# Optimization experiments

Measured on AMD Instinct MI355X. Metric: run time of the kernel, lower is better.

## Reference

```python
import math
import jax, jax.numpy as jnp
import numpy as np

P = 8; K = 9; RC = 8; FC = 768; TOPK = 2
THR = 0.2; TEMP = 0.08; DIL = 5; MIX = 0.65; OPEN = 5


def _build_bank():
    axis = np.linspace(-1.0, 1.0, K, dtype=np.float32)
    yy, xx = np.meshgrid(axis, axis, indexing='ij')
    Ls = [0.45, 0.75, 1.05]; Ws = [0.14, 0.2, 0.28]
    kernels, oris, lens, wids = [], [], [], []
    for i in range(P):
        ang = 2.0 * math.pi * i / P
        L = Ls[i % 3]; W = Ws[(i // 3) % 3]
        xr = xx * math.cos(ang) + yy * math.sin(ang)
        yr = -xx * math.sin(ang) + yy * math.cos(ang)
        taper = (1.0 - np.clip(np.abs(xr) / L, 0.0, 1.0)) ** 1.5
        core = np.exp(-0.5 * ((xr / L) ** 2 + (yr / W) ** 2))
        ridge = taper * core * np.clip(1.0 - (yr / W) ** 2, 0.0, None)
        k = ridge - ridge.mean()
        k = k / max(np.abs(k).sum(), 1e-6)
        kernels.append(k.astype(np.float32)); oris.append(ang); lens.append(L); wids.append(W)
    return (jnp.asarray(np.stack(kernels)[:, None]),
            jnp.asarray(np.array(oris, np.float32)),
            jnp.asarray(np.array(lens, np.float32)),
            jnp.asarray(np.array(wids, np.float32)))


def _conv(x, w, b, pad):
    y = jax.lax.conv_general_dilated(x, w, (1, 1), [(pad, pad), (pad, pad)],
                                     dimension_numbers=('NCHW', 'OIHW', 'NCHW'))
    return y + b[None, :, None, None]


def _avg3(x):  # torch avg_pool2d k=3,s=1,p=1 with count_include_pad=True -> sum/9
    s = jax.lax.reduce_window(x, 0.0, jax.lax.add, (1, 1, 3, 3), (1, 1, 1, 1),
                              [(0, 0), (0, 0), (1, 1), (1, 1)])
    return s / 9.0


def _maxp(x, k):
    p = k // 2
    return jax.lax.reduce_window(x, -jnp.inf, jax.lax.max, (1, 1, k, k), (1, 1, 1, 1),
                                 [(0, 0), (0, 0), (p, p), (p, p)])


def _binary_open(mask, k):
    eroded = 1.0 - _maxp(1.0 - mask, k)
    return jnp.clip(_maxp(eroded, k), 0.0, 1.0)


def _normalize(t):
    mn = t.min(axis=(-2, -1), keepdims=True)
    mx = t.max(axis=(-2, -1), keepdims=True)
    return (t - mn) / jnp.maximum(mx - mn, 1e-6)


def _gelu(x):
    return jax.nn.gelu(x, approximate=False)


def _forward(feature_map, theta, length, width, curvature, alpha, objectness,
             prototype_logits, fp1_w, fp1_b, fp2_w, fp2_b, pm1_w, pm1_b,
             pm2_w, pm2_b, proto_delta):
    bank, ori, la, wa = _build_bank()
    carrier = _gelu(_conv(_gelu(_conv(feature_map, fp1_w, fp1_b, 0)), fp2_w, fp2_b, 1))
    carrier_mean = carrier.mean(axis=1, keepdims=True)
    carrier_hp = carrier_mean - _avg3(carrier_mean)
    kernels = bank + 0.05 * proto_delta
    responses = jax.lax.conv_general_dilated(carrier_hp, kernels, (1, 1),
                                             [(K // 2, K // 2)] * 2,
                                             dimension_numbers=('NCHW', 'OIHW', 'NCHW'))
    theta_angle = jnp.tanh(theta) * math.pi  # [B,1,H,W]
    theta_score = jnp.cos(theta_angle - ori[None, :, None, None])
    length_value = jax.nn.sigmoid(length) * 0.85 + 0.25
    width_value = jax.nn.sigmoid(width) * 0.22 + 0.08
    length_score = -(length_value - la[None, :, None, None]) ** 2 / 0.08
    width_score = -(width_value - wa[None, :, None, None]) ** 2 / 0.01
    bias = prototype_logits + 1.25 * theta_score + length_score + width_score
    pw = jax.nn.softmax(bias, axis=1)  # [B,P,H,W]
    # per-pixel top-k prototype selection
    pwt = jnp.moveaxis(pw, 1, -1)  # [B,H,W,P]
    vals, idx = jax.lax.top_k(pwt, TOPK)
    sparse = (jax.nn.one_hot(idx, P, dtype=pw.dtype) * vals[..., None]).sum(axis=-2)
    sparse = sparse / jnp.maximum(sparse.sum(axis=-1, keepdims=True), 1e-6)
    pw = jnp.moveaxis(sparse, -1, 1)
    alpha_map = jax.nn.sigmoid(alpha)
    objectness_map = jax.nn.sigmoid(objectness)
    curvature_map = jnp.tanh(curvature)
    ss = (responses * pw).sum(axis=1, keepdims=True)
    ss = ss - _avg3(ss)
    density = jnp.abs(carrier).mean(axis=1, keepdims=True)
    density = density / jnp.maximum(density.mean(axis=(2, 3), keepdims=True), 1e-6)
    dx = jnp.cos(theta_angle); dy = jnp.sin(theta_angle)
    blob = _avg3(objectness_map)
    # support gating (enabled, hard-mask + opening)
    carrier_support = _normalize(_avg3(jnp.abs(carrier_hp)))
    density_support = _normalize(density)
    ev = MIX * carrier_support + (1.0 - MIX) * density_support
    gate = jax.nn.sigmoid((ev - THR) / TEMP)
    gate = _maxp(gate, DIL)
    mask = (ev >= THR).astype(feature_map.dtype)
    mask = _binary_open(mask, OPEN)
    mask = _maxp(mask, DIL)
    gate = gate * mask
    blob = blob * jax.lax.stop_gradient(gate)
    stroke_gate = alpha_map * blob * (0.7 + 0.3 * jnp.clip(density, 0.0, 2.0))
    ss = stroke_gate * ss * (1.0 + 0.15 * curvature_map)
    feats = jnp.concatenate([carrier * ss, ss, dx * ss, dy * ss, curvature_map * ss], axis=1)  # [B,RC+4,H,W]
    h = _gelu(_conv(feats, pm1_w, pm1_b, 0))
    return _conv(h, pm2_w, pm2_b, 0)  # [B,FC,H,W]


def setup_inputs() -> dict:
    key = jax.random.key(0)
    ks = jax.random.split(key, 16)
    B, H, W = 8, 64, 64
    n = lambda k, s: jax.random.normal(k, s, dtype=jnp.float32)
    return {
        'feature_map': n(ks[0], (B, FC, H, W)),
        'theta': n(ks[1], (B, 1, H, W)),
        'length': n(ks[2], (B, 1, H, W)),
        'width': n(ks[3], (B, 1, H, W)),
        'curvature': n(ks[4], (B, 1, H, W)),
        'alpha': n(ks[5], (B, 1, H, W)),
        'objectness': n(ks[6], (B, 1, H, W)),
        'prototype_logits': n(ks[7], (B, P, H, W)),
        'fp1_w': n(ks[8], (RC, FC, 1, 1)) * 0.02,
        'fp1_b': jnp.zeros((RC,), jnp.float32),
        'fp2_w': n(ks[9], (RC, RC, 3, 3)) * 0.05,
        'fp2_b': jnp.zeros((RC,), jnp.float32),
        'pm1_w': n(ks[10], (RC, RC + 4, 1, 1)) * 0.05,
        'pm1_b': jnp.zeros((RC,), jnp.float32),
        'pm2_w': n(ks[11], (FC, RC, 1, 1)) * 0.05,
        'pm2_b': jnp.zeros((FC,), jnp.float32),
        'proto_delta': n(ks[12], (P, 1, K, K)) * 0.02,
    }


def reference(feature_map, theta, length, width, curvature, alpha, objectness,
              prototype_logits, fp1_w, fp1_b, fp2_w, fp2_b, pm1_w, pm1_b,
              pm2_w, pm2_b, proto_delta):
    return _forward(feature_map, theta, length, width, curvature, alpha, objectness,
                    prototype_logits, fp1_w, fp1_b, fp2_w, fp2_b, pm1_w, pm1_b,
                    pm2_w, pm2_b, proto_delta)
```

## Files before the change

### kernel.cpp

```cpp
#include <hip/hip_runtime.h>
#include <math.h>

#define PI_F 3.14159265358979323846f

__device__ __forceinline__ float gelu_f(float x){ return 0.5f*x*(1.0f+erff(x*0.7071067811865475f)); }
__device__ __forceinline__ float sigm_f(float x){ return 1.0f/(1.0f+expf(-x)); }

typedef float nf4 __attribute__((ext_vector_type(4)));
__device__ __forceinline__ float4 nt_load4(const float4* p){
    nf4 v = __builtin_nontemporal_load((const nf4*)p);
    return make_float4(v.x, v.y, v.z, v.w);
}
__device__ __forceinline__ void nt_store4(float4* p, float4 v){
    nf4 w; w.x=v.x; w.y=v.y; w.z=v.z; w.w=v.w;
    __builtin_nontemporal_store(w, (nf4*)p);
}


__global__ void __launch_bounds__(256) k_conv1(const float* __restrict__ fm,
                        const float* __restrict__ w1, const float* __restrict__ pd,
                        float* __restrict__ part, float* __restrict__ klg){
    int chunk = blockIdx.x;
    int g = blockIdx.y;
    int tid = threadIdx.x;
    __shared__ float wl[96*8];
    __shared__ float4 comb[8][128];
    for (int i=tid;i<768;i+=256){ int c=i>>3, co=i&7; wl[i]=w1[co*768 + g*96 + c]; }
    __syncthreads();
    int b = chunk>>3;
    int f4 = tid&127, half = tid>>7;
    int q0 = ((chunk&7)<<7) + f4;
    const float4* fm4 = (const float4*)fm;
    float4 acc[8];
    #pragma unroll
    for(int co=0;co<8;co++) acc[co]=make_float4(0.f,0.f,0.f,0.f);
    int basec = b*768 + g*96 + half*48;
    #pragma unroll 4
    for(int c=0;c<48;c++){
        float4 x = nt_load4(&fm4[(size_t)(basec+c)*1024 + q0]);
        int ch = half*48 + c;
        #pragma unroll
        for(int co=0;co<8;co++){
            float wv = wl[(ch<<3)+co];
            acc[co].x += wv*x.x; acc[co].y += wv*x.y; acc[co].z += wv*x.z; acc[co].w += wv*x.w;
        }
    }
    if(half==1){
        #pragma unroll
        for(int co=0;co<8;co++) comb[co][f4]=acc[co];
    }
    __syncthreads();
    if(half==0){
        float4* p4 = (float4*)part;
        int gq = (b<<10) + q0;
        #pragma unroll
        for(int co=0;co<8;co++){
            float4 o = comb[co][f4];
            o.x+=acc[co].x; o.y+=acc[co].y; o.z+=acc[co].z; o.w+=acc[co].w;
            p4[(size_t)((g<<3)+co)*8192 + gq] = o;
        }
    }

    if(chunk==0 && g==0){
        __shared__ float ridge[648];
        __shared__ float pmS[8], pdenS[8];
        for(int t=tid;t<648;t+=256){
            int p=t/81, idx=t-p*81;
            int i=idx/9, j=idx-i*9;
            float ay=-1.f+0.25f*(float)i;
            float ax=-1.f+0.25f*(float)j;
            float ang=2.f*PI_F*(float)p*0.125f;
            const float Ls[3]={0.45f,0.75f,1.05f};
            const float Ws[3]={0.14f,0.20f,0.28f};
            float L=Ls[p%3], Wd=Ws[(p/3)%3];
            float cs=cosf(ang), sn=sinf(ang);
            float xr=ax*cs+ay*sn;
            float yr=-ax*sn+ay*cs;
            float tp=1.f-fminf(fabsf(xr)/L,1.f);
            float taper=powf(tp,1.5f);
            float core=expf(-0.5f*((xr/L)*(xr/L)+(yr/Wd)*(yr/Wd)));
            ridge[t]=taper*core*fmaxf(1.f-(yr/Wd)*(yr/Wd),0.f);
        }
        __syncthreads();
        {
            int p=tid>>5, k=tid&31;
            float s=0.f;
            for(int e=k;e<81;e+=32) s+=ridge[p*81+e];
            for(int off=16;off>0;off>>=1) s+=__shfl_down(s,off,32);
            if(k==0) pmS[p]=s*(1.f/81.f);
        }
        __syncthreads();
        {
            int p=tid>>5, k=tid&31;
            float m=pmS[p];
            float s=0.f;
            for(int e=k;e<81;e+=32) s+=fabsf(ridge[p*81+e]-m);
            for(int off=16;off>0;off>>=1) s+=__shfl_down(s,off,32);
            if(k==0) pdenS[p]=fmaxf(s,1e-6f);
        }
        __syncthreads();
        for(int t=tid;t<648;t+=256){
            int p=t/81;
            klg[t]=(ridge[t]-pmS[p])/pdenS[p]+0.05f*pd[t];
        }
    }
}

__global__ void __launch_bounds__(256) k_conv2(const float* __restrict__ part,
    const float* __restrict__ b1, const float* __restrict__ w2, const float* __restrict__ b2,
    float* __restrict__ carrier, float* __restrict__ cm, float* __restrict__ absc,
    float* __restrict__ bpart){
    __shared__ float t1T[8][3][64];
    __shared__ float w2s[576];
    __shared__ float b1s[8];
    __shared__ float sumS[4][64];
    __shared__ float saS[4][64];
    int tid=threadIdx.x, bl=blockIdx.x;
    int b=bl>>6, y=bl&63;
    for(int i=tid;i<576;i+=256) w2s[i]=w2[i];
    if(tid<8) b1s[tid]=b1[tid];
    __syncthreads();
    for(int j=tid;j<1536;j+=256){
        int ci=j/192, rem=j-ci*192, r=rem>>6, x=rem&63;
        int gy=y-1+r;
        float v=0.f;
        if(gy>=0 && gy<64){
            int px=(b<<12)+(gy<<6)+x;
            float s=0.f;
            #pragma unroll
            for(int g=0;g<8;g++) s+=part[(size_t)((g<<3)+ci)*32768+px];
            v=gelu_f(s+b1s[ci]);
        }
        t1T[ci][r][x]=v;
    }
    __syncthreads();
    int x=tid&63, cg=tid>>6;
    float acc[2];
    #pragma unroll
    for(int qq=0;qq<2;qq++) acc[qq]=b2[cg*2+qq];
    for(int ci=0;ci<8;ci++){
        #pragma unroll
        for(int r=0;r<3;r++){
            #pragma unroll
            for(int dx=-1;dx<=1;dx++){
                int xx=x+dx;
                float v=(xx>=0&&xx<64)?t1T[ci][r][xx]:0.f;
                int ti=r*3+(dx+1);
                #pragma unroll
                for(int qq=0;qq<2;qq++) acc[qq]+=v*w2s[(((cg*2+qq)*8+ci)*9)+ti];
            }
        }
    }
    float s2=0.f, sa2=0.f;
    #pragma unroll
    for(int qq=0;qq<2;qq++){
        float cv=gelu_f(acc[qq]);
        carrier[((size_t)((b<<3)+cg*2+qq)<<12)+(y<<6)+x]=cv;
        s2+=cv; sa2+=fabsf(cv);
    }
    sumS[cg][x]=s2; saS[cg][x]=sa2;
    __syncthreads();
    if(cg==0){
        float cmv=(sumS[0][x]+sumS[1][x]+sumS[2][x]+sumS[3][x])*0.125f;
        float av =(saS[0][x]+saS[1][x]+saS[2][x]+saS[3][x])*0.125f;
        int gp=(b<<12)+(y<<6)+x;
        cm[gp]=cmv;
        absc[gp]=av;
        float s=av, mn=av, mx=av;
        #pragma unroll
        for(int off=32;off>0;off>>=1){
            s += __shfl_down(s,off);
            mn = fminf(mn,__shfl_down(mn,off));
            mx = fmaxf(mx,__shfl_down(mx,off));
        }
        if(x==0){
            bpart[bl*8+0]=s;
            bpart[bl*8+3]=mn;
            bpart[bl*8+4]=mx;
        }
    }
}

__global__ void __launch_bounds__(256) k_resp(const float* __restrict__ cm,
    const float* __restrict__ klg, const float* __restrict__ theta,
    const float* __restrict__ length, const float* __restrict__ width,
    const float* __restrict__ plog,
    float* __restrict__ csraw, float* __restrict__ ss0, float* __restrict__ bpart){
    __shared__ float cmT[704];
    __shared__ float chpT[576];
    __shared__ float klS[648];
    __shared__ float mg[64][16];
    int tid=threadIdx.x, bl=blockIdx.x;
    int b=bl>>6, y=bl&63;
    for(int i=tid;i<648;i+=256) klS[i]=klg[i];
    for(int j=tid;j<704;j+=256){
        int r=j>>6, x=j&63;
        int gy=y-5+r;
        cmT[j]=(gy>=0&&gy<64)?cm[(b<<12)+(gy<<6)+x]:0.f;
    }
    __syncthreads();
    for(int j=tid;j<576;j+=256){
        int rh=j>>6, x=j&63;
        int gy=y-4+rh;
        float v=0.f;
        if(gy>=0&&gy<64){
            float s=0.f;
            #pragma unroll
            for(int dy=0;dy<3;dy++){
                #pragma unroll
                for(int dx=-1;dx<=1;dx++){
                    int xx=x+dx;
                    if(xx>=0&&xx<64) s+=cmT[(rh+dy)*64+xx];
                }
            }
            v=cmT[(rh+1)*64+x]-s*(1.f/9.f);
        }
        chpT[j]=v;
    }
    __syncthreads();
    int x=tid&63, qg=tid>>6;
    int gp=(b<<12)+(y<<6)+x;
    float acc[2]={0.f,0.f};
    float cs=0.f;
    for(int dy=-4;dy<=4;dy++){
        int lr=dy+4;
        for(int dx=-4;dx<=4;dx++){
            int xx=x+dx;
            float v=(xx>=0&&xx<64)?chpT[lr*64+xx]:0.f;
            int ti=lr*9+(dx+4);
            acc[0]+=v*klS[(qg*2)*81+ti];
            acc[1]+=v*klS[(qg*2+1)*81+ti];
            if(qg==0 && dy>=-1&&dy<=1&&dx>=-1&&dx<=1) cs+=fabsf(v);
        }
    }
    float ta=tanhf(theta[gp])*PI_F;
    float lv=sigm_f(length[gp])*0.85f+0.25f;
    float wv=sigm_f(width[gp])*0.22f+0.08f;
    const float Ls[3]={0.45f,0.75f,1.05f};
    const float Ws[3]={0.14f,0.20f,0.28f};
    int pp=(y<<6)+x;
    float bias[2];
    #pragma unroll
    for(int qq=0;qq<2;qq++){
        int q=qg*2+qq;
        float ang=2.f*PI_F*(float)q*0.125f;
        float la=Ls[q%3], wa=Ws[(q/3)%3];
        bias[qq]=plog[((size_t)((b<<3)+q)<<12)+pp]
               +1.25f*cosf(ta-ang)
               -(lv-la)*(lv-la)*(1.f/0.08f)
               -(wv-wa)*(wv-wa)*(1.f/0.01f);
    }
    float m1,r1,m2,r2;
    if(bias[1]>bias[0]){ m1=bias[1];r1=acc[1]; m2=bias[0];r2=acc[0]; }
    else               { m1=bias[0];r1=acc[0]; m2=bias[1];r2=acc[1]; }
    mg[x][qg*4+0]=m1; mg[x][qg*4+1]=r1; mg[x][qg*4+2]=m2; mg[x][qg*4+3]=r2;
    __syncthreads();
    if(qg==0){
        float M1=mg[x][0],R1=mg[x][1],M2=mg[x][2],R2=mg[x][3];
        #pragma unroll
        for(int g=1;g<4;g++){
            float m1b=mg[x][g*4],r1b=mg[x][g*4+1],m2b=mg[x][g*4+2],r2b=mg[x][g*4+3];
            if(m1b>M1){
                float nM2,nR2;
                if(m2b>M1){nM2=m2b;nR2=r2b;} else {nM2=M1;nR2=R1;}
                M1=m1b;R1=r1b;M2=nM2;R2=nR2;
            } else if(m1b>M2){
                M2=m1b;R2=r1b;
            }
        }
        float e2=expf(M2-M1);
        float inv=1.0f/(1.0f+e2);
        ss0[gp]=R1*inv + R2*e2*inv;
        float csv=cs*(1.f/9.f);
        csraw[gp]=csv;
        float mn=csv, mx=csv;
        #pragma unroll
        for(int off=32;off>0;off>>=1){
            mn=fminf(mn,__shfl_down(mn,off));
            mx=fmaxf(mx,__shfl_down(mx,off));
        }
        if(x==0){
            bpart[bl*8+1]=mn;
            bpart[bl*8+2]=mx;
        }
    }
}

__global__ void __launch_bounds__(256) k_gate(const float* __restrict__ csraw,
    const float* __restrict__ absc, const float* __restrict__ objn,
    const float* __restrict__ alpha, const float* __restrict__ bpart,
    float* __restrict__ sg){
    __shared__ float evT[1280];
    __shared__ float gmT[1280];
    __shared__ float eT[1024];
    __shared__ float m1T[768];
    __shared__ float obT[640];
    __shared__ float red5[5];
    int blk=blockIdx.x, tid=threadIdx.x;
    int b=blk>>3, y0=(blk&7)<<3;
    if(tid==0){
        float sm=0.f, cmn=1e30f, cmx=-1e30f, amn=1e30f, amx=-1e30f;
        for(int j=0;j<64;j++){
            const float* bp=&bpart[(b*64+j)*8];
            sm+=bp[0];
            cmn=fminf(cmn,bp[1]); cmx=fmaxf(cmx,bp[2]);
            amn=fminf(amn,bp[3]); amx=fmaxf(amx,bp[4]);
        }
        float den=fmaxf(sm*(1.0f/4096.0f),1e-6f);
        red5[0]=den; red5[1]=cmn; red5[2]=cmx; red5[3]=amn/den; red5[4]=amx/den;
    }
    __syncthreads();
    float den=red5[0], cmn=red5[1], dmn=red5[3];
    float cinv = 1.0f/fmaxf(red5[2]-cmn,1e-6f);
    float dinv = 1.0f/fmaxf(red5[4]-dmn,1e-6f);
    for(int j=tid;j<1280;j+=256){
        int r=j>>6, x=j&63; int gy=y0-6+r;
        float ev=0.f;
        if(gy>=0&&gy<64){
            int gp=(b<<12)+(gy<<6)+x;
            float cs=(csraw[gp]-cmn)*cinv;
            float d=absc[gp]/den;
            ev=0.65f*cs+0.35f*((d-dmn)*dinv);
        }
        evT[j]=ev;
        gmT[j]=sigm_f((ev-0.2f)*(1.0f/0.08f));
    }
    for(int j=tid;j<640;j+=256){
        int r=j>>6,x=j&63; int gy=y0-1+r;
        obT[j]=(gy>=0&&gy<64)?sigm_f(objn[(b<<12)+(gy<<6)+x]):0.f;
    }
    __syncthreads();
    for(int j=tid;j<1024;j+=256){
        int r=j>>6,x=j&63; int gy=y0-4+r;
        float m=0.f;
        if(gy>=0&&gy<64){
            m=1.f;
            for(int dy=-2;dy<=2;dy++){int yy=gy+dy; if(yy<0||yy>=64)continue;
                int lr=yy-(y0-6);
                for(int dx=-2;dx<=2;dx++){int xx=x+dx; if(xx<0||xx>=64)continue;
                    if(evT[(lr<<6)+xx]<0.2f) m=0.f;}}
        }
        eT[j]=m;
    }
    __syncthreads();
    for(int j=tid;j<768;j+=256){
        int r=j>>6,x=j&63; int gy=y0-2+r;
        float m=0.f;
        if(gy>=0&&gy<64){
            m=-1e30f;
            for(int dy=-2;dy<=2;dy++){int yy=gy+dy; if(yy<0||yy>=64)continue;
                int lr=yy-(y0-4);
                for(int dx=-2;dx<=2;dx++){int xx=x+dx; if(xx<0||xx>=64)continue;
                    m=fmaxf(m,eT[(lr<<6)+xx]);}}
        }
        m1T[j]=m;
    }
    __syncthreads();
    for(int k=0;k<2;k++){
        int p=tid+(k<<8);
        int ly=p>>6, x=p&63; int gy=y0+ly;
        int gp=(b<<12)+(gy<<6)+x;
        float m2=-1e30f, gx=-1e30f;
        for(int dy=-2;dy<=2;dy++){int yy=gy+dy; if(yy<0||yy>=64)continue;
            int lr1=yy-(y0-2), lr2=yy-(y0-6);
            for(int dx=-2;dx<=2;dx++){int xx=x+dx; if(xx<0||xx>=64)continue;
                m2=fmaxf(m2,m1T[(lr1<<6)+xx]);
                gx=fmaxf(gx,gmT[(lr2<<6)+xx]);}}
        float s=0.f;
        for(int dy=-1;dy<=1;dy++){int yy=gy+dy; if(yy<0||yy>=64)continue;
            int lr=yy-(y0-1);
            for(int dx=-1;dx<=1;dx++){int xx=x+dx; if(xx<0||xx>=64)continue;
                s+=obT[(lr<<6)+xx];}}
        float blob=s*(1.0f/9.0f);
        float gate=gx*m2;
        float d=absc[gp]/den;
        sg[gp]=sigm_f(alpha[gp])*blob*gate*(0.7f+0.3f*fminf(fmaxf(d,0.f),2.f));
    }
}

__global__ void __launch_bounds__(256) k_out(const float* __restrict__ ss0,
    const float* __restrict__ sg, const float* __restrict__ theta,
    const float* __restrict__ curv, const float* __restrict__ carrier,
    const float* __restrict__ w3, const float* __restrict__ b3,
    const float* __restrict__ w4, const float* __restrict__ b4,
    float* __restrict__ out){
    __shared__ float hS[8][64];
    __shared__ float w4s[768*8];
    __shared__ float b4s[768];
    __shared__ float wl[96];
    __shared__ float bl3[8];
    int tid=threadIdx.x;
    int bln=blockIdx.x;
    for(int i=tid;i<6144;i+=256) w4s[i]=w4[i];
    for(int i=tid;i<768;i+=256) b4s[i]=b4[i];
    if(tid<96) wl[tid]=w3[tid];
    if(tid<8) bl3[tid]=b3[tid];
    __syncthreads();

    if(tid<64){
        int gp=bln*64+tid;
        int b=gp>>12, p=gp&4095, y=p>>6, x=p&63;
        const float* base = ss0 + (b<<12);
        float s=0.f;
        for(int dy=-1;dy<=1;dy++){int yy=y+dy; if(yy<0||yy>=64)continue;
            for(int dx=-1;dx<=1;dx++){int xx=x+dx;if(xx<0||xx>=64)continue;
                s+=base[(yy<<6)+xx];}}
        float ss1 = base[p]-s*(1.0f/9.0f);
        float cu = tanhf(curv[gp]);
        float ssv = sg[gp]*ss1*(1.0f+0.15f*cu);
        float ta = tanhf(theta[gp])*PI_F;
        float dxv=cosf(ta), dyv=sinf(ta);
        float car[8];
        #pragma unroll
        for(int ci=0;ci<8;ci++) car[ci]=carrier[((size_t)((b<<3)+ci)<<12)+p];
        #pragma unroll
        for(int co=0;co<8;co++){
            const float* w=&wl[co*12];
            float t = w[8] + w[9]*dxv + w[10]*dyv + w[11]*cu;
            #pragma unroll
            for(int ci=0;ci<8;ci++) t += w[ci]*car[ci];
            hS[co][tid] = gelu_f(bl3[co] + ssv*t);
        }
    }
    __syncthreads();

    int px4 = tid&15;
    int cg = tid>>4;
    int q0 = bln*16 + px4;
    int b = q0>>10;
    int ql = q0 & 1023;
    float4 hv[8];
    #pragma unroll
    for(int ci=0;ci<8;ci++) hv[ci]=*(const float4*)&hS[ci][px4<<2];
    float4* o4=(float4*)out;
    for(int k=0;k<48;k++){
        int co=cg*48+k;
        float bb=b4s[co];
        float4 o=make_float4(bb,bb,bb,bb);
        const float* w=&w4s[co<<3];
        #pragma unroll
        for(int ci=0;ci<8;ci++){
            float wv=w[ci];
            o.x+=wv*hv[ci].x; o.y+=wv*hv[ci].y; o.z+=wv*hv[ci].z; o.w+=wv*hv[ci].w;
        }
        nt_store4(&o4[(size_t)(b*768+co)*1024 + ql], o);
    }
}

extern "C" void kernel_launch(void* const* d_in, const int* in_sizes, int n_in,
                              void* d_out, int out_size, void* d_ws, size_t ws_size,
                              hipStream_t stream) {
    const float* fm     =(const float*)d_in[0];
    const float* theta  =(const float*)d_in[1];
    const float* length =(const float*)d_in[2];
    const float* width  =(const float*)d_in[3];
    const float* curv   =(const float*)d_in[4];
    const float* alpha  =(const float*)d_in[5];
    const float* objn   =(const float*)d_in[6];
    const float* plog   =(const float*)d_in[7];
    const float* fp1w   =(const float*)d_in[8];
    const float* fp1b   =(const float*)d_in[9];
    const float* fp2w   =(const float*)d_in[10];
    const float* fp2b   =(const float*)d_in[11];
    const float* pm1w   =(const float*)d_in[12];
    const float* pm1b   =(const float*)d_in[13];
    const float* pm2w   =(const float*)d_in[14];
    const float* pm2b   =(const float*)d_in[15];
    const float* pdelta =(const float*)d_in[16];

    float* ws=(float*)d_ws;
    float* part    = ws;
    float* carrier = part + 2097152;
    float* absc    = carrier + 262144;
    float* csraw   = absc + 32768;
    float* ss0     = csraw + 32768;
    float* sg      = ss0 + 32768;
    float* cm      = sg + 32768;
    float* bpart   = cm + 32768;
    float* klg     = bpart + 4096;
    float* out     = (float*)d_out;

    k_conv1<<<dim3(64,8), 256, 0, stream>>>(fm, fp1w, pdelta, part, klg);
    k_conv2<<<512, 256, 0, stream>>>(part, fp1b, fp2w, fp2b, carrier, cm, absc, bpart);
    k_resp <<<512, 256, 0, stream>>>(cm, klg, theta, length, width, plog,
                                     csraw, ss0, bpart);
    k_gate <<<64, 256, 0, stream>>>(csraw, absc, objn, alpha, bpart, sg);
    k_out  <<<512, 256, 0, stream>>>(ss0, sg, theta, curv, carrier,
                                     pm1w, pm1b, pm2w, pm2b, out);
}
```

Baseline: 281.7 us.

## Fuse channel reduction into conv1 and merge gate computation into output kernel

```diff
diff --git a/kernel.cpp b/kernel.cpp
--- a/kernel.cpp
+++ b/kernel.cpp
@@ -18,50 +18,52 @@
 
 
 __global__ void __launch_bounds__(256) k_conv1(const float* __restrict__ fm,
-                        const float* __restrict__ w1, const float* __restrict__ pd,
-                        float* __restrict__ part, float* __restrict__ klg){
-    int chunk = blockIdx.x;
-    int g = blockIdx.y;
+                        const float* __restrict__ w1, const float* __restrict__ b1,
+                        const float* __restrict__ pd,
+                        float* __restrict__ t1, float* __restrict__ klg){
+    __shared__ float wl[768*8];
+    __shared__ float4 pT[16][8][16];
+    int bln = blockIdx.x;
     int tid = threadIdx.x;
-    __shared__ float wl[96*8];
-    __shared__ float4 comb[8][128];
-    for (int i=tid;i<768;i+=256){ int c=i>>3, co=i&7; wl[i]=w1[co*768 + g*96 + c]; }
-    __syncthreads();
-    int b = chunk>>3;
-    int f4 = tid&127, half = tid>>7;
-    int q0 = ((chunk&7)<<7) + f4;
+    int b = bln>>6;
+    int q4base = (bln&63)<<4;
+    for (int i=tid;i<6144;i+=256){ int c=i>>3, co=i&7; wl[i]=w1[co*768 + c]; }
+    __syncthreads();
+    int f4i = tid&15, grp = tid>>4;
+    int q4 = q4base + f4i;
     const float4* fm4 = (const float4*)fm;
     float4 acc[8];
     #pragma unroll
     for(int co=0;co<8;co++) acc[co]=make_float4(0.f,0.f,0.f,0.f);
-    int basec = b*768 + g*96 + half*48;
+    int ch0 = grp*48;
     #pragma unroll 4
     for(int c=0;c<48;c++){
-        float4 x = nt_load4(&fm4[(size_t)(basec+c)*1024 + q0]);
-        int ch = half*48 + c;
+        int ch = ch0 + c;
+        float4 x = nt_load4(&fm4[(size_t)(b*768 + ch)*1024 + q4]);
         #pragma unroll
         for(int co=0;co<8;co++){
             float wv = wl[(ch<<3)+co];
             acc[co].x += wv*x.x; acc[co].y += wv*x.y; acc[co].z += wv*x.z; acc[co].w += wv*x.w;
         }
     }
-    if(half==1){
-        #pragma unroll
-        for(int co=0;co<8;co++) comb[co][f4]=acc[co];
-    }
-    __syncthreads();
-    if(half==0){
-        float4* p4 = (float4*)part;
-        int gq = (b<<10) + q0;
-        #pragma unroll
-        for(int co=0;co<8;co++){
-            float4 o = comb[co][f4];
-            o.x+=acc[co].x; o.y+=acc[co].y; o.z+=acc[co].z; o.w+=acc[co].w;
-            p4[(size_t)((g<<3)+co)*8192 + gq] = o;
-        }
-    }
-
-    if(chunk==0 && g==0){
+    #pragma unroll
+    for(int co=0;co<8;co++) pT[grp][co][f4i]=acc[co];
+    __syncthreads();
+    if(tid<128){
+        int co=tid>>4, fi=tid&15;
+        float4 s=make_float4(0.f,0.f,0.f,0.f);
+        #pragma unroll
+        for(int g=0;g<16;g++){
+            float4 v=pT[g][co][fi];
+            s.x+=v.x; s.y+=v.y; s.z+=v.z; s.w+=v.w;
+        }
+        float bb=b1[co];
+        float4 o;
+        o.x=gelu_f(s.x+bb); o.y=gelu_f(s.y+bb); o.z=gelu_f(s.z+bb); o.w=gelu_f(s.w+bb);
+        ((float4*)t1)[(size_t)co*8192 + (b<<10) + q4base + fi] = o;
+    }
+
+    if(bln==0){
         __shared__ float ridge[648];
         __shared__ float pmS[8], pdenS[8];
         for(int t=tid;t<648;t+=256){
@@ -106,30 +108,23 @@
     }
 }
 
-__global__ void __launch_bounds__(256) k_conv2(const float* __restrict__ part,
-    const float* __restrict__ b1, const float* __restrict__ w2, const float* __restrict__ b2,
+__global__ void __launch_bounds__(256) k_conv2(const float* __restrict__ t1,
+    const float* __restrict__ w2, const float* __restrict__ b2,
     float* __restrict__ carrier, float* __restrict__ cm, float* __restrict__ absc,
     float* __restrict__ bpart){
     __shared__ float t1T[8][3][64];
     __shared__ float w2s[576];
-    __shared__ float b1s[8];
     __shared__ float sumS[4][64];
     __shared__ float saS[4][64];
     int tid=threadIdx.x, bl=blockIdx.x;
     int b=bl>>6, y=bl&63;
     for(int i=tid;i<576;i+=256) w2s[i]=w2[i];
-    if(tid<8) b1s[tid]=b1[tid];
-    __syncthreads();
     for(int j=tid;j<1536;j+=256){
         int ci=j/192, rem=j-ci*192, r=rem>>6, x=rem&63;
         int gy=y-1+r;
         float v=0.f;
         if(gy>=0 && gy<64){
-            int px=(b<<12)+(gy<<6)+x;
-            float s=0.f;
-            #pragma unroll
-            for(int g=0;g<8;g++) s+=part[(size_t)((g<<3)+ci)*32768+px];
-            v=gelu_f(s+b1s[ci]);
+            v = t1[(size_t)ci*32768 + (b<<12)+(gy<<6)+x];
         }
         t1T[ci][r][x]=v;
     }
@@ -286,35 +281,54 @@
     }
 }
 
-__global__ void __launch_bounds__(256) k_gate(const float* __restrict__ csraw,
-    const float* __restrict__ absc, const float* __restrict__ objn,
-    const float* __restrict__ alpha, const float* __restrict__ bpart,
-    float* __restrict__ sg){
-    __shared__ float evT[1280];
-    __shared__ float gmT[1280];
-    __shared__ float eT[1024];
-    __shared__ float m1T[768];
-    __shared__ float obT[640];
+__global__ void __launch_bounds__(256) k_out(const float* __restrict__ ss0,
+    const float* __restrict__ csraw, const float* __restrict__ absc,
+    const float* __restrict__ objn, const float* __restrict__ alpha,
+    const float* __restrict__ theta, const float* __restrict__ curv,
+    const float* __restrict__ carrier, const float* __restrict__ bpart,
+    const float* __restrict__ w3, const float* __restrict__ b3,
+    const float* __restrict__ w4, const float* __restrict__ b4,
+    float* __restrict__ out){
+    __shared__ float hS[8][64];
+    __shared__ float w4s[768*8];
+    __shared__ float b4s[768];
+    __shared__ float wl3[96];
+    __shared__ float bl3[8];
+    __shared__ float evT[13*64];
+    __shared__ float gmT[13*64];
+    __shared__ float eT[9*64];
+    __shared__ float m1T[5*64];
+    __shared__ float obT[3*64];
     __shared__ float red5[5];
-    int blk=blockIdx.x, tid=threadIdx.x;
-    int b=blk>>3, y0=(blk&7)<<3;
-    if(tid==0){
-        float sm=0.f, cmn=1e30f, cmx=-1e30f, amn=1e30f, amx=-1e30f;
-        for(int j=0;j<64;j++){
-            const float* bp=&bpart[(b*64+j)*8];
-            sm+=bp[0];
-            cmn=fminf(cmn,bp[1]); cmx=fmaxf(cmx,bp[2]);
-            amn=fminf(amn,bp[3]); amx=fmaxf(amx,bp[4]);
-        }
-        float den=fmaxf(sm*(1.0f/4096.0f),1e-6f);
-        red5[0]=den; red5[1]=cmn; red5[2]=cmx; red5[3]=amn/den; red5[4]=amx/den;
+    int tid=threadIdx.x;
+    int bln=blockIdx.x;
+    int b=bln>>6, y=bln&63;
+    for(int i=tid;i<6144;i+=256) w4s[i]=w4[i];
+    for(int i=tid;i<768;i+=256) b4s[i]=b4[i];
+    if(tid<96) wl3[tid]=w3[tid];
+    if(tid<8) bl3[tid]=b3[tid];
+    if(tid<64){
+        const float* bp=&bpart[((size_t)b*64+tid)*8];
+        float sm=bp[0], cmn=bp[1], cmx=bp[2], amn=bp[3], amx=bp[4];
+        #pragma unroll
+        for(int off=32;off>0;off>>=1){
+            sm  += __shfl_down(sm,off);
+            cmn  = fminf(cmn,__shfl_down(cmn,off));
+            cmx  = fmaxf(cmx,__shfl_down(cmx,off));
+            amn  = fminf(amn,__shfl_down(amn,off));
+            amx  = fmaxf(amx,__shfl_down(amx,off));
+        }
+        if(tid==0){
+            float den=fmaxf(sm*(1.0f/4096.0f),1e-6f);
+            red5[0]=den; red5[1]=cmn; red5[2]=cmx; red5[3]=amn/den; red5[4]=amx/den;
+        }
     }
     __syncthreads();
     float den=red5[0], cmn=red5[1], dmn=red5[3];
     float cinv = 1.0f/fmaxf(red5[2]-cmn,1e-6f);
     float dinv = 1.0f/fmaxf(red5[4]-dmn,1e-6f);
-    for(int j=tid;j<1280;j+=256){
-        int r=j>>6, x=j&63; int gy=y0-6+r;
+    for(int j=tid;j<832;j+=256){
+        int r=j>>6, x=j&63; int gy=y-6+r;
         float ev=0.f;
         if(gy>=0&&gy<64){
             int gp=(b<<12)+(gy<<6)+x;
@@ -325,97 +339,71 @@
         evT[j]=ev;
         gmT[j]=sigm_f((ev-0.2f)*(1.0f/0.08f));
     }
-    for(int j=tid;j<640;j+=256){
-        int r=j>>6,x=j&63; int gy=y0-1+r;
+    for(int j=tid;j<192;j+=256){
+        int r=j>>6,x=j&63; int gy=y-1+r;
         obT[j]=(gy>=0&&gy<64)?sigm_f(objn[(b<<12)+(gy<<6)+x]):0.f;
     }
     __syncthreads();
-    for(int j=tid;j<1024;j+=256){
-        int r=j>>6,x=j&63; int gy=y0-4+r;
+    for(int j=tid;j<576;j+=256){
+        int r=j>>6,x=j&63; int gy=y-4+r;
         float m=0.f;
         if(gy>=0&&gy<64){
             m=1.f;
             for(int dy=-2;dy<=2;dy++){int yy=gy+dy; if(yy<0||yy>=64)continue;
-                int lr=yy-(y0-6);
+                int lr=yy-(y-6);
                 for(int dx=-2;dx<=2;dx++){int xx=x+dx; if(xx<0||xx>=64)continue;
                     if(evT[(lr<<6)+xx]<0.2f) m=0.f;}}
         }
         eT[j]=m;
     }
     __syncthreads();
-    for(int j=tid;j<768;j+=256){
-        int r=j>>6,x=j&63; int gy=y0-2+r;
+    for(int j=tid;j<320;j+=256){
+        int r=j>>6,x=j&63; int gy=y-2+r;
         float m=0.f;
         if(gy>=0&&gy<64){
             m=-1e30f;
             for(int dy=-2;dy<=2;dy++){int yy=gy+dy; if(yy<0||yy>=64)continue;
-                int lr=yy-(y0-4);
+                int lr=yy-(y-4);
                 for(int dx=-2;dx<=2;dx++){int xx=x+dx; if(xx<0||xx>=64)continue;
                     m=fmaxf(m,eT[(lr<<6)+xx]);}}
         }
         m1T[j]=m;
     }
     __syncthreads();
-    for(int k=0;k<2;k++){
-        int p=tid+(k<<8);
-        int ly=p>>6, x=p&63; int gy=y0+ly;
-        int gp=(b<<12)+(gy<<6)+x;
+    if(tid<64){
+        int x=tid;
+        int gp=(b<<12)+(y<<6)+x;
         float m2=-1e30f, gx=-1e30f;
-        for(int dy=-2;dy<=2;dy++){int yy=gy+dy; if(yy<0||yy>=64)continue;
-            int lr1=yy-(y0-2), lr2=yy-(y0-6);
+        for(int dy=-2;dy<=2;dy++){int yy=y+dy; if(yy<0||yy>=64)continue;
+            int lr1=yy-(y-2), lr2=yy-(y-6);
             for(int dx=-2;dx<=2;dx++){int xx=x+dx; if(xx<0||xx>=64)continue;
                 m2=fmaxf(m2,m1T[(lr1<<6)+xx]);
                 gx=fmaxf(gx,gmT[(lr2<<6)+xx]);}}
         float s=0.f;
-        for(int dy=-1;dy<=1;dy++){int yy=gy+dy; if(yy<0||yy>=64)continue;
-            int lr=yy-(y0-1);
+        for(int dy=-1;dy<=1;dy++){int yy=y+dy; if(yy<0||yy>=64)continue;
+            int lr=yy-(y-1);
             for(int dx=-1;dx<=1;dx++){int xx=x+dx; if(xx<0||xx>=64)continue;
                 s+=obT[(lr<<6)+xx];}}
         float blob=s*(1.0f/9.0f);
         float gate=gx*m2;
         float d=absc[gp]/den;
-        sg[gp]=sigm_f(alpha[gp])*blob*gate*(0.7f+0.3f*fminf(fmaxf(d,0.f),2.f));
-    }
-}
-
-__global__ void __launch_bounds__(256) k_out(const float* __restrict__ ss0,
-    const float* __restrict__ sg, const float* __restrict__ theta,
-    const float* __restrict__ curv, const float* __restrict__ carrier,
-    const float* __restrict__ w3, const float* __restrict__ b3,
-    const float* __restrict__ w4, const float* __restrict__ b4,
-    float* __restrict__ out){
-    __shared__ float hS[8][64];
-    __shared__ float w4s[768*8];
-    __shared__ float b4s[768];
-    __shared__ float wl[96];
-    __shared__ float bl3[8];
-    int tid=threadIdx.x;
-    int bln=blockIdx.x;
-    for(int i=tid;i<6144;i+=256) w4s[i]=w4[i];
-    for(int i=tid;i<768;i+=256) b4s[i]=b4[i];
-    if(tid<96) wl[tid]=w3[tid];
-    if(tid<8) bl3[tid]=b3[tid];
-    __syncthreads();
-
-    if(tid<64){
-        int gp=bln*64+tid;
-        int b=gp>>12, p=gp&4095, y=p>>6, x=p&63;
+        float sgv=sigm_f(alpha[gp])*blob*gate*(0.7f+0.3f*fminf(fmaxf(d,0.f),2.f));
         const float* base = ss0 + (b<<12);
-        float s=0.f;
+        float ssum=0.f;
         for(int dy=-1;dy<=1;dy++){int yy=y+dy; if(yy<0||yy>=64)continue;
             for(int dx=-1;dx<=1;dx++){int xx=x+dx;if(xx<0||xx>=64)continue;
-                s+=base[(yy<<6)+xx];}}
-        float ss1 = base[p]-s*(1.0f/9.0f);
+                ssum+=base[(yy<<6)+xx];}}
+        float ss1 = base[(y<<6)+x]-ssum*(1.0f/9.0f);
         float cu = tanhf(curv[gp]);
-        float ssv = sg[gp]*ss1*(1.0f+0.15f*cu);
+        float ssv = sgv*ss1*(1.0f+0.15f*cu);
         float ta = tanhf(theta[gp])*PI_F;
         float dxv=cosf(ta), dyv=sinf(ta);
         float car[8];
         #pragma unroll
-        for(int ci=0;ci<8;ci++) car[ci]=carrier[((size_t)((b<<3)+ci)<<12)+p];
+        for(int ci=0;ci<8;ci++) car[ci]=carrier[((size_t)((b<<3)+ci)<<12)+(y<<6)+x];
         #pragma unroll
         for(int co=0;co<8;co++){
-            const float* w=&wl[co*12];
+            const float* w=&wl3[co*12];
             float t = w[8] + w[9]*dxv + w[10]*dyv + w[11]*cu;
             #pragma unroll
             for(int ci=0;ci<8;ci++) t += w[ci]*car[ci];
@@ -423,11 +411,10 @@
         }
     }
     __syncthreads();
-
     int px4 = tid&15;
     int cg = tid>>4;
     int q0 = bln*16 + px4;
-    int b = q0>>10;
+    int bb_ = q0>>10;
     int ql = q0 & 1023;
     float4 hv[8];
     #pragma unroll
@@ -435,15 +422,15 @@
     float4* o4=(float4*)out;
     for(int k=0;k<48;k++){
         int co=cg*48+k;
-        float bb=b4s[co];
-        float4 o=make_float4(bb,bb,bb,bb);
+        float bv=b4s[co];
+        float4 o=make_float4(bv,bv,bv,bv);
         const float* w=&w4s[co<<3];
         #pragma unroll
         for(int ci=0;ci<8;ci++){
             float wv=w[ci];
             o.x+=wv*hv[ci].x; o.y+=wv*hv[ci].y; o.z+=wv*hv[ci].z; o.w+=wv*hv[ci].w;
         }
-        nt_store4(&o4[(size_t)(b*768+co)*1024 + ql], o);
+        nt_store4(&o4[(size_t)(bb_*768+co)*1024 + ql], o);
     }
 }
 
@@ -469,22 +456,20 @@
     const float* pdelta =(const float*)d_in[16];
 
     float* ws=(float*)d_ws;
-    float* part    = ws;
-    float* carrier = part + 2097152;
+    float* t1      = ws;
+    float* carrier = t1 + 262144;
     float* absc    = carrier + 262144;
     float* csraw   = absc + 32768;
     float* ss0     = csraw + 32768;
-    float* sg      = ss0 + 32768;
-    float* cm      = sg + 32768;
+    float* cm      = ss0 + 32768;
     float* bpart   = cm + 32768;
     float* klg     = bpart + 4096;
     float* out     = (float*)d_out;
 
-    k_conv1<<<dim3(64,8), 256, 0, stream>>>(fm, fp1w, pdelta, part, klg);
-    k_conv2<<<512, 256, 0, stream>>>(part, fp1b, fp2w, fp2b, carrier, cm, absc, bpart);
+    k_conv1<<<512, 256, 0, stream>>>(fm, fp1w, fp1b, pdelta, t1, klg);
+    k_conv2<<<512, 256, 0, stream>>>(t1, fp2w, fp2b, carrier, cm, absc, bpart);
     k_resp <<<512, 256, 0, stream>>>(cm, klg, theta, length, width, plog,
                                      csraw, ss0, bpart);
-    k_gate <<<64, 256, 0, stream>>>(csraw, absc, objn, alpha, bpart, sg);
-    k_out  <<<512, 256, 0, stream>>>(ss0, sg, theta, curv, carrier,
-                                     pm1w, pm1b, pm2w, pm2b, out);
-}
+    k_out  <<<512, 256, 0, stream>>>(ss0, csraw, absc, objn, alpha, theta, curv,
+                                     carrier, bpart, pm1w, pm1b, pm2w, pm2b, out);
+}
```

Measured after the change: 246.0 us. -12.7%, faster.
